# Kernel tuning notes

Measured on AMD Instinct MI355X. Metric: run time of the kernel, lower is better.

## Reference

```python
import jax, jax.numpy as jnp
import numpy as np


def _bilinear(x, py, px):
    # x: [B,C,H,W]; py,px: [B,K,Ho,Wo] fractional sample coords (zero pad outside)
    B, C, H, W = x.shape
    K, Ho, Wo = py.shape[1], py.shape[2], py.shape[3]
    xf = x.reshape(B, C, H * W)
    y0 = jnp.floor(py)
    x0 = jnp.floor(px)

    def gather(yi, xi):
        valid = (yi >= 0) & (yi <= H - 1) & (xi >= 0) & (xi <= W - 1)
        yc = jnp.clip(yi, 0, H - 1).astype(jnp.int32)
        xc = jnp.clip(xi, 0, W - 1).astype(jnp.int32)
        idx = (yc * W + xc).reshape(B, 1, -1)  # [B,1,K*Ho*Wo]
        v = jnp.take_along_axis(xf, idx, axis=2)  # [B,C,K*Ho*Wo]
        return v * valid.reshape(B, 1, -1)

    wy1 = (py - y0).reshape(B, 1, -1)
    wx1 = (px - x0).reshape(B, 1, -1)
    wy0 = 1.0 - wy1
    wx0 = 1.0 - wx1
    v = (gather(y0, x0) * (wy0 * wx0)
         + gather(y0, x0 + 1) * (wy0 * wx1)
         + gather(y0 + 1, x0) * (wy1 * wx0)
         + gather(y0 + 1, x0 + 1) * (wy1 * wx1))
    return v.reshape(B, C, K, Ho, Wo)


def _deform_merge(x, w_off, b_off, w_def, gamma, beta):
    B, C, H, W = x.shape
    Co = w_def.shape[0]
    K, stride = 4, 2  # 2x2 kernel
    Ho, Wo = H // 2, W // 2
    # offset-predicting conv (same k/s/p as deform conv): [B, 2K, Ho, Wo]
    off = jax.lax.conv_general_dilated(x, w_off, (stride, stride), 'VALID')
    off = off + b_off[None, :, None, None]
    off = off.reshape(B, K, 2, Ho, Wo)  # (dy, dx) per kernel tap
    ky = jnp.arange(K) // 2
    kx = jnp.arange(K) % 2
    base_y = (jnp.arange(Ho) * stride)[None, None, :, None] + ky[None, :, None, None]
    base_x = (jnp.arange(Wo) * stride)[None, None, None, :] + kx[None, :, None, None]
    py = base_y.astype(x.dtype) + off[:, :, 0]
    px = base_x.astype(x.dtype) + off[:, :, 1]
    sampled = _bilinear(x, py, px)  # [B,C,K,Ho,Wo]
    y = jnp.einsum('bckhw,ock->bohw', sampled, w_def.reshape(Co, C, K))
    # BatchNorm2d (training-mode batch stats, eps=1e-5) + exact GELU
    mu = y.mean(axis=(0, 2, 3), keepdims=True)
    var = y.var(axis=(0, 2, 3), keepdims=True)
    yn = (y - mu) * jax.lax.rsqrt(var + 1e-5)
    yn = yn * gamma[None, :, None, None] + beta[None, :, None, None]
    yg = jax.nn.gelu(yn, approximate=False)
    return yg.reshape(B, Co, Ho * Wo).transpose(0, 2, 1)  # [B, L/4, Co]


def setup_inputs() -> dict:
    key = jax.random.key(0)
    k0, k1, k2 = jax.random.split(key, 3)
    B, C, H, W, Co = 16, 96, 112, 112, 192
    x = jax.random.normal(k0, (B, C, H, W), jnp.float32)
    # conv_offset: 2*kh*kw = 8 output channels (zero-init in mmcv; small random here)
    w_off = jax.random.normal(k1, (8, C, 2, 2), jnp.float32) * 0.01
    b_off = jnp.zeros((8,), jnp.float32)
    w_def = jax.random.normal(k2, (Co, C, 2, 2), jnp.float32) * (1.0 / np.sqrt(C * 4))
    gamma = jnp.ones((Co,), jnp.float32)
    beta = jnp.zeros((Co,), jnp.float32)
    return {"x": x, "h": H, "w": W, "w_off": w_off, "b_off": b_off,
            "w_def": w_def, "gamma": gamma, "beta": beta}


def reference(x, h, w, w_off, b_off, w_def, gamma, beta):
    assert x.shape[2] == h and x.shape[3] == w
    return _deform_merge(x, w_off, b_off, w_def, gamma, beta)
```

## Files before the change

### kernel.cpp

```cpp
#include <hip/hip_runtime.h>
#include <math.h>

#define BB 16
#define CC 96
#define HH 112
#define WW 112
#define HO 56
#define WO 56
#define LL (HO*WO)
#define CO 192
#define CKD 384
#define NPIX (BB*LL)

#define TPX 28
#define CHK 8
#define NCHUNK 12
#define WROWS 4
#define WCOLS 64
#define WSTRIDE 260
#define APAD 40
#define OSTRIDE 228

#define WS_SSUM  16
#define WS_SSQS  208
#define WS_B_OFF 4096
#define B_ELEMS  73728
#define WS_SOFF_OFF 299008
#define SOFF_BYTES (BB*HO*WO*8*4)

typedef short bf16x8 __attribute__((ext_vector_type(8)));
typedef float f32x4  __attribute__((ext_vector_type(4)));

__device__ __forceinline__ void split8(const float4 a0, const float4 a1,
                                       bf16x8& hi, bf16x8& lo)
{
    float f[8] = {a0.x, a0.y, a0.z, a0.w, a1.x, a1.y, a1.z, a1.w};
    #pragma unroll
    for (int j = 0; j < 8; ++j) {
        unsigned bits = __float_as_uint(f[j]);
        float fh = __uint_as_float(bits & 0xFFFF0000u);
        float fl = f[j] - fh;
        hi[j] = (short)(bits >> 16);
        lo[j] = (short)(__float_as_uint(fl) >> 16);
    }
}

__global__ void k_zero(float* __restrict__ ws) {
    int t = threadIdx.x;
    if (t < 384) ws[WS_SSUM + t] = 0.f;
}

__global__ void k_prep(const float* __restrict__ w_def,
                       unsigned short* __restrict__ bhi,
                       unsigned short* __restrict__ blo,
                       float* __restrict__ ws)
{
    if (blockIdx.x == 0 && threadIdx.x < 384) ws[WS_SSUM + threadIdx.x] = 0.f;
    int t = blockIdx.x * 256 + threadIdx.x;
    if (t >= 12 * 12 * 64) return;
    int ln  = t & 63;
    int ks  = (t >> 6) % 12;
    int ntg = t / (64 * 12);
    int n  = ntg * 16 + (ln & 15);
    int k0 = ks * 32 + (ln >> 4) * 8;
    const float* wp = w_def + (size_t)n * CKD + k0;
    #pragma unroll
    for (int j = 0; j < 8; ++j) {
        float f = wp[j];
        unsigned bits = __float_as_uint(f);
        float fh = __uint_as_float(bits & 0xFFFF0000u);
        float fl = f - fh;
        bhi[t * 8 + j] = (unsigned short)(bits >> 16);
        blo[t * 8 + j] = (unsigned short)(__float_as_uint(fl) >> 16);
    }
}

__global__ __launch_bounds__(512) void k_pre(
    const float* __restrict__ x, const float* __restrict__ w_off,
    const float* __restrict__ b_off, const float* __restrict__ w_def,
    unsigned short* __restrict__ bhi, unsigned short* __restrict__ blo,
    float* __restrict__ soff_all, float* __restrict__ ws)
{
    __shared__ float win[CHK * OSTRIDE];
    const int blk = blockIdx.x;
    const int tid = threadIdx.x;

    if (blk < 18) {
        if (blk == 0 && tid < 384) ws[WS_SSUM + tid] = 0.f;
        int t = blk * 512 + tid;
        int ln  = t & 63;
        int ks  = (t >> 6) % 12;
        int ntg = t / (64 * 12);
        int n  = ntg * 16 + (ln & 15);
        int k0 = ks * 32 + (ln >> 4) * 8;
        const float* wp = w_def + (size_t)n * CKD + k0;
        #pragma unroll
        for (int j = 0; j < 8; ++j) {
            float f = wp[j];
            unsigned bits = __float_as_uint(f);
            float fh = __uint_as_float(bits & 0xFFFF0000u);
            float fl = f - fh;
            bhi[t * 8 + j] = (unsigned short)(bits >> 16);
            blo[t * 8 + j] = (unsigned short)(__float_as_uint(fl) >> 16);
        }
        return;
    }

    const int bb = blk - 18;
    const int oy = bb % HO;
    const int b  = bb / HO;
    const int iy = oy * 2;
    const int pix = tid >> 3, och = tid & 7;
    const int c_s = tid / 56, u_s = tid % 56;
    const int r_s = u_s / 28, q_s = u_s % 28;
    float dacc = 0.f;

    float4 v0, v1, v2;
    #define OFF_LD(CH) (*(const float4*)(x + (((size_t)(b*CC + (CH)*CHK + c_s)*HH) + iy + r_s)*WW + q_s*4))
    if (tid < 448) { v0 = OFF_LD(0); v1 = OFF_LD(1); v2 = OFF_LD(2); }

    #define OFF_STEP(CH, VB) \
        __syncthreads(); \
        if (tid < 448) { \
            *(float4*)&win[c_s*OSTRIDE + r_s*112 + q_s*4] = VB; \
            if ((CH) + 3 < NCHUNK) VB = OFF_LD((CH) + 3); \
        } \
        __syncthreads(); \
        if (tid < 448) { \
            const float* wb = w_off + (size_t)och*(CC*4) + (CH)*CHK*4; \
            _Pragma("unroll") \
            for (int c = 0; c < CHK; ++c) { \
                float2 t0 = *(const float2*)&win[c*OSTRIDE + 2*pix]; \
                float2 t1 = *(const float2*)&win[c*OSTRIDE + 112 + 2*pix]; \
                float4 a = *(const float4*)(wb + c*4); \
                dacc += t0.x*a.x + t0.y*a.y + t1.x*a.z + t1.y*a.w; \
            } \
        }

    #pragma unroll
    for (int g = 0; g < 4; ++g) {
        OFF_STEP(3*g + 0, v0)
        OFF_STEP(3*g + 1, v1)
        OFF_STEP(3*g + 2, v2)
    }
    #undef OFF_STEP
    #undef OFF_LD

    if (tid < 448)
        soff_all[((size_t)(b*HO + oy)*WO)*8 + tid] = dacc + b_off[och];
}

__global__ __launch_bounds__(512, 8) void k_main8(
    const float* __restrict__ x,
    const unsigned short* __restrict__ bhi, const unsigned short* __restrict__ blo,
    const float* __restrict__ soff_all,
    float* __restrict__ yout, float* __restrict__ ws)
{
    __shared__ float win[CHK * WSTRIDE];
    __shared__ unsigned short smAh[32 * APAD];
    __shared__ unsigned short smAl[32 * APAD];
    __shared__ float soff[TPX * 8];

    const int tid = threadIdx.x;
    const int b  = blockIdx.y;
    const int bx = blockIdx.x;
    const int oy  = bx >> 1;
    const int ox0 = (bx & 1) * TPX;
    const int iy  = oy * 2;
    const int ix0 = ox0 * 2;
    const int ln = tid & 63;
    const int w  = tid >> 6;
    const int wr = w & 1;
    const int wc = w >> 1;
    const int row0 = ln & 15;
    const int kg   = ln >> 4;

    if (tid < 128) {
        int rr = 28 + (tid >> 5), cc = tid & 31;
        smAh[rr*APAD + cc] = 0;
        smAl[rr*APAD + cc] = 0;
    }
    if (tid < 56) {
        const float* sp = soff_all + ((size_t)(b*HO + oy)*WO + ox0)*8;
        *(float4*)&soff[tid*4] = *(const float4*)(sp + tid*4);
    }

    const int cg  = tid & 15;
    const int pr  = tid >> 4;
    const int sr  = pr & 3;
    const int scn = pr >> 2;
    const int skk = tid & 31;
    const int sc  = skk >> 2;
    const int sk  = skk & 3;
    const int sky = sk >> 1, skx = sk & 1;
    const int wr0 = iy - 1, wc0 = ix0 - 4;

    auto stage_ld = [&](int ch) -> float4 {
        int gr = min(max(wr0 + sr, 0), HH - 1);
        int gc0 = wc0 + cg * 4;
        const float* src = x + (((size_t)(b*CC + ch*CHK + scn)*HH) + gr)*WW;
        float4 v;
        if (gc0 >= 0 && gc0 <= WW - 4) {
            v = *(const float4*)(src + gc0);
        } else {
            v.x = src[min(max(gc0 + 0, 0), WW - 1)];
            v.y = src[min(max(gc0 + 1, 0), WW - 1)];
            v.z = src[min(max(gc0 + 2, 0), WW - 1)];
            v.w = src[min(max(gc0 + 3, 0), WW - 1)];
        }
        return v;
    };
    float* wdst = &win[scn*WSTRIDE + sr*WCOLS + cg*4];

    f32x4 acc[3];
    #pragma unroll
    for (int nt = 0; nt < 3; ++nt) acc[nt] = (f32x4){0.f, 0.f, 0.f, 0.f};

    float4 vst = stage_ld(NCHUNK - 1);
    *(float4*)wdst = vst;
    vst = stage_ld(NCHUNK - 2);

    for (int ch = NCHUNK - 1; ch >= 0; --ch) {
        __syncthreads();
        {
            const float* xc = x + ((size_t)(b*CC + ch*CHK + sc)*HH)*WW;
            const float* wchan = &win[sc*WSTRIDE];
            #pragma unroll
            for (int j = 0; j < 2; ++j) {
                int pix = (tid >> 5) + 16 * j;
                if (pix < TPX) {
                    float2 so = *(const float2*)&soff[pix*8 + 2*sk];
                    float fy = (float)(iy + sky) + so.x;
                    float fx = (float)(ix0 + 2*pix + skx) + so.y;
                    float y0f = floorf(fy), x0f = floorf(fx);
                    int y0 = (int)y0f, x0 = (int)x0f;
                    float wy1 = fy - y0f, wx1 = fx - x0f;
                    float wy0 = 1.f - wy1, wx0 = 1.f - wx1;
                    int y1 = y0 + 1, x1 = x0 + 1;
                    bool vy0 = (y0 >= 0) && (y0 <= HH - 1);
                    bool vy1 = (y1 >= 0) && (y1 <= HH - 1);
                    bool vx0 = (x0 >= 0) && (x0 <= WW - 1);
                    bool vx1 = (x1 >= 0) && (x1 <= WW - 1);
                    int cy0 = min(max(y0, 0), HH - 1), cy1 = min(max(y1, 0), HH - 1);
                    int cx0 = min(max(x0, 0), WW - 1), cx1 = min(max(x1, 0), WW - 1);
                    float w00 = (vy0 && vx0) ? wy0 * wx0 : 0.f;
                    float w01 = (vy0 && vx1) ? wy0 * wx1 : 0.f;
                    float w10 = (vy1 && vx0) ? wy1 * wx0 : 0.f;
                    float w11 = (vy1 && vx1) ? wy1 * wx1 : 0.f;
                    int ry0 = cy0 - wr0, ry1 = cy1 - wr0;
                    int rx0 = cx0 - wc0, rx1 = cx1 - wc0;
                    bool inw = ((unsigned)ry0 <= (unsigned)(WROWS - 1)) &&
                               ((unsigned)ry1 <= (unsigned)(WROWS - 1)) &&
                               ((unsigned)rx0 <= (unsigned)(WCOLS - 1)) &&
                               ((unsigned)rx1 <= (unsigned)(WCOLS - 1));
                    float v;
                    if (inw) {
                        v = w00 * wchan[ry0*WCOLS + rx0] + w01 * wchan[ry0*WCOLS + rx1]
                          + w10 * wchan[ry1*WCOLS + rx0] + w11 * wchan[ry1*WCOLS + rx1];
                    } else {
                        v = w00 * xc[cy0*WW + cx0] + w01 * xc[cy0*WW + cx1]
                          + w10 * xc[cy1*WW + cx0] + w11 * xc[cy1*WW + cx1];
                    }
                    unsigned u = __float_as_uint(v);
                    float fh = __uint_as_float(u & 0xFFFF0000u);
                    smAh[pix*APAD + skk] = (unsigned short)(u >> 16);
                    smAl[pix*APAD + skk] = (unsigned short)(__float_as_uint(v - fh) >> 16);
                }
            }
        }
        __syncthreads();
        bf16x8 ah = *(const bf16x8*)&smAh[(wr*16 + row0)*APAD + kg*8];
        bf16x8 al = *(const bf16x8*)&smAl[(wr*16 + row0)*APAD + kg*8];
        #pragma unroll
        for (int nt = 0; nt < 3; ++nt) {
            size_t idx = ((size_t)(((wc*3 + nt)*12 + ch)*64) + ln)*8;
            bf16x8 bh = *(const bf16x8*)(bhi + idx);
            bf16x8 bl = *(const bf16x8*)(blo + idx);
            acc[nt] = __builtin_amdgcn_mfma_f32_16x16x32_bf16(ah, bh, acc[nt], 0, 0, 0);
            acc[nt] = __builtin_amdgcn_mfma_f32_16x16x32_bf16(ah, bl, acc[nt], 0, 0, 0);
            acc[nt] = __builtin_amdgcn_mfma_f32_16x16x32_bf16(al, bh, acc[nt], 0, 0, 0);
        }
        if (ch > 0) *(float4*)wdst = vst;
        if (ch > 1) vst = stage_ld(ch - 2);
    }

    #pragma unroll
    for (int nt = 0; nt < 3; ++nt) {
        float s = 0.f, q = 0.f;
        #pragma unroll
        for (int r = 0; r < 4; ++r) {
            float v = acc[nt][r];
            s += v; q += v * v;
        }
        s += __shfl_xor(s, 16); s += __shfl_xor(s, 32);
        q += __shfl_xor(q, 16); q += __shfl_xor(q, 32);
        if (ln < 16) {
            atomicAdd(&ws[WS_SSUM + wc*48 + nt*16 + ln], s);
            atomicAdd(&ws[WS_SSQS + wc*48 + nt*16 + ln], q);
        }
    }
    size_t obase = (size_t)b * LL + (size_t)oy * WO + ox0;
    #pragma unroll
    for (int r = 0; r < 4; ++r) {
        int pp = wr*16 + kg*4 + r;
        if (pp < TPX) {
            float* dst = yout + (obase + pp)*CO + wc*48 + row0;
            dst[0]  = acc[0][r];
            dst[16] = acc[1][r];
            dst[32] = acc[2][r];
        }
    }
}

template<bool PREP>
__device__ __forceinline__ void tile_body(
    const float* __restrict__ x, const float* __restrict__ w_off,
    const float* __restrict__ b_off, const float* __restrict__ w_def,
    const unsigned short* __restrict__ bhi, const unsigned short* __restrict__ blo,
    float* win, unsigned short* smAh, unsigned short* smAl, float* soff,
    int b, int bx, int tid, f32x4 (&acc)[2][3])
{
    const int oy  = bx >> 1;
    const int ox0 = (bx & 1) * TPX;
    const int iy  = oy * 2;
    const int ix0 = ox0 * 2;
    const int ln = tid & 63;
    const int w  = tid >> 6;

    float dacc = 0.f;
    const int cpix = tid >> 3;
    const int coch = tid & 7;
    const int spair = tid / 14;
    const int sq    = tid % 14;
    for (int ch = 0; ch < NCHUNK; ++ch) {
        __syncthreads();
        if (tid < 224) {
            int c = spair >> 1, r = spair & 1;
            const float* src = x + (((size_t)(b*CC + ch*CHK + c)*HH) + iy + r)*WW + ix0 + sq*4;
            *(float4*)&win[(c*2 + r)*56 + sq*4] = *(const float4*)src;
        }
        __syncthreads();
        if (tid < 224) {
            const float* wb = w_off + (size_t)coch*(CC*4) + ch*CHK*4;
            #pragma unroll
            for (int c = 0; c < CHK; ++c) {
                float2 t0 = *(const float2*)&win[(c*2 + 0)*56 + 2*cpix];
                float2 t1 = *(const float2*)&win[(c*2 + 1)*56 + 2*cpix];
                float4 a = *(const float4*)(wb + c*4);
                dacc += t0.x*a.x + t0.y*a.y + t1.x*a.z + t1.y*a.w;
            }
        }
    }
    if (tid < 224) soff[cpix*8 + coch] = dacc + b_off[coch];

    const int row0 = ln & 15;
    const int kg   = ln >> 4;
    const int skk = tid & 31;
    const int sc  = skk >> 2;
    const int sk  = skk & 3;
    const int sky = sk >> 1, skx = sk & 1;
    const int wr0 = iy - 1, wc0 = ix0 - 4;

    for (int ch = NCHUNK - 1; ch >= 0; --ch) {
        __syncthreads();
        #pragma unroll
        for (int j = 0; j < 2; ++j) {
            int li = tid + 256*j;
            int cg = li & 15;
            int pr = li >> 4;
            int r = pr & 3, c = pr >> 2;
            int gr = min(max(wr0 + r, 0), HH - 1);
            int gc0 = wc0 + cg*4;
            const float* src = x + (((size_t)(b*CC + ch*CHK + c)*HH) + gr)*WW;
            float4 v;
            if (gc0 >= 0 && gc0 <= WW - 4) {
                v = *(const float4*)(src + gc0);
            } else {
                v.x = src[min(max(gc0 + 0, 0), WW - 1)];
                v.y = src[min(max(gc0 + 1, 0), WW - 1)];
                v.z = src[min(max(gc0 + 2, 0), WW - 1)];
                v.w = src[min(max(gc0 + 3, 0), WW - 1)];
            }
            *(float4*)&win[c*WSTRIDE + r*WCOLS + cg*4] = v;
        }
        __syncthreads();
        {
            const float* xc = x + ((size_t)(b*CC + ch*CHK + sc)*HH)*WW;
            const float* wchan = &win[sc*WSTRIDE];
            #pragma unroll
            for (int j = 0; j < 4; ++j) {
                if (j < 3 || tid < 128) {
                    int pix = (tid >> 5) + 8*j;
                    float2 so = *(const float2*)&soff[pix*8 + 2*sk];
                    float fy = (float)(iy + sky) + so.x;
                    float fx = (float)(ix0 + 2*pix + skx) + so.y;
                    float y0f = floorf(fy), x0f = floorf(fx);
                    int y0 = (int)y0f, x0 = (int)x0f;
                    float wy1 = fy - y0f, wx1 = fx - x0f;
                    float wy0 = 1.f - wy1, wx0 = 1.f - wx1;
                    int y1 = y0 + 1, x1 = x0 + 1;
                    bool vy0 = (y0 >= 0) && (y0 <= HH - 1);
                    bool vy1 = (y1 >= 0) && (y1 <= HH - 1);
                    bool vx0 = (x0 >= 0) && (x0 <= WW - 1);
                    bool vx1 = (x1 >= 0) && (x1 <= WW - 1);
                    int cy0 = min(max(y0, 0), HH - 1), cy1 = min(max(y1, 0), HH - 1);
                    int cx0 = min(max(x0, 0), WW - 1), cx1 = min(max(x1, 0), WW - 1);
                    float w00 = (vy0 && vx0) ? wy0*wx0 : 0.f;
                    float w01 = (vy0 && vx1) ? wy0*wx1 : 0.f;
                    float w10 = (vy1 && vx0) ? wy1*wx0 : 0.f;
                    float w11 = (vy1 && vx1) ? wy1*wx1 : 0.f;
                    int ry0 = cy0 - wr0, ry1 = cy1 - wr0;
                    int rx0 = cx0 - wc0, rx1 = cx1 - wc0;
                    bool inw = ((unsigned)ry0 <= (unsigned)(WROWS - 1)) &&
                               ((unsigned)ry1 <= (unsigned)(WROWS - 1)) &&
                               ((unsigned)rx0 <= (unsigned)(WCOLS - 1)) &&
                               ((unsigned)rx1 <= (unsigned)(WCOLS - 1));
                    float v;
                    if (inw) {
                        v = w00*wchan[ry0*WCOLS + rx0] + w01*wchan[ry0*WCOLS + rx1]
                          + w10*wchan[ry1*WCOLS + rx0] + w11*wchan[ry1*WCOLS + rx1];
                    } else {
                        v = w00*xc[cy0*WW + cx0] + w01*xc[cy0*WW + cx1]
                          + w10*xc[cy1*WW + cx0] + w11*xc[cy1*WW + cx1];
                    }
                    unsigned u = __float_as_uint(v);
                    float fh = __uint_as_float(u & 0xFFFF0000u);
                    smAh[pix*APAD + skk] = (unsigned short)(u >> 16);
                    smAl[pix*APAD + skk] = (unsigned short)(__float_as_uint(v - fh) >> 16);
                }
            }
        }
        __syncthreads();
        bf16x8 ah[2], al[2];
        #pragma unroll
        for (int mt = 0; mt < 2; ++mt) {
            ah[mt] = *(const bf16x8*)&smAh[(mt*16 + row0)*APAD + kg*8];
            al[mt] = *(const bf16x8*)&smAl[(mt*16 + row0)*APAD + kg*8];
        }
        #pragma unroll
        for (int nt = 0; nt < 3; ++nt) {
            bf16x8 bh, bl;
            if (PREP) {
                size_t idx = ((size_t)(((w*3 + nt)*12 + ch)*64) + ln)*8;
                bh = *(const bf16x8*)(bhi + idx);
                bl = *(const bf16x8*)(blo + idx);
            } else {
                const float* wp = w_def + (size_t)(w*48 + nt*16 + row0)*CKD + ch*32 + kg*8;
                float4 b0 = *(const float4*)wp;
                float4 b1 = *(const float4*)(wp + 4);
                split8(b0, b1, bh, bl);
            }
            #pragma unroll
            for (int mt = 0; mt < 2; ++mt) {
                acc[mt][nt] = __builtin_amdgcn_mfma_f32_16x16x32_bf16(ah[mt], bh, acc[mt][nt], 0, 0, 0);
                acc[mt][nt] = __builtin_amdgcn_mfma_f32_16x16x32_bf16(ah[mt], bl, acc[mt][nt], 0, 0, 0);
                acc[mt][nt] = __builtin_amdgcn_mfma_f32_16x16x32_bf16(al[mt], bh, acc[mt][nt], 0, 0, 0);
            }
        }
    }
}

template<bool PREP>
__global__ __launch_bounds__(256, 4) void k_main_r3(
    const float* __restrict__ x, const float* __restrict__ w_off,
    const float* __restrict__ b_off, const float* __restrict__ w_def,
    const unsigned short* __restrict__ bhi, const unsigned short* __restrict__ blo,
    float* __restrict__ yout, float* __restrict__ ws)
{
    __shared__ float win[CHK * WSTRIDE];
    __shared__ unsigned short smAh[32 * APAD];
    __shared__ unsigned short smAl[32 * APAD];
    __shared__ float soff[TPX * 8];

    const int tid = threadIdx.x;
    const int b  = blockIdx.y;
    const int bx = blockIdx.x;
    const int ln = tid & 63;
    const int w  = tid >> 6;
    const int row0 = ln & 15;
    const int kg   = ln >> 4;

    if (tid < 128) {
        int rr = 28 + (tid >> 5), cc = tid & 31;
        smAh[rr*APAD + cc] = 0;
        smAl[rr*APAD + cc] = 0;
    }

    f32x4 acc[2][3];
    #pragma unroll
    for (int mt = 0; mt < 2; ++mt)
        #pragma unroll
        for (int nt = 0; nt < 3; ++nt)
            acc[mt][nt] = (f32x4){0.f, 0.f, 0.f, 0.f};

    tile_body<PREP>(x, w_off, b_off, w_def, bhi, blo,
                    win, smAh, smAl, soff, b, bx, tid, acc);

    #pragma unroll
    for (int nt = 0; nt < 3; ++nt) {
        float s = 0.f, q = 0.f;
        #pragma unroll
        for (int mt = 0; mt < 2; ++mt)
            #pragma unroll
            for (int r = 0; r < 4; ++r) {
                float v = acc[mt][nt][r];
                s += v; q += v * v;
            }
        s += __shfl_xor(s, 16); s += __shfl_xor(s, 32);
        q += __shfl_xor(q, 16); q += __shfl_xor(q, 32);
        if (ln < 16) {
            atomicAdd(&ws[WS_SSUM + w*48 + nt*16 + ln], s);
            atomicAdd(&ws[WS_SSQS + w*48 + nt*16 + ln], q);
        }
    }
    int oy = bx >> 1, ox0 = (bx & 1)*TPX;
    size_t obase = (size_t)b*LL + (size_t)oy*WO + ox0;
    #pragma unroll
    for (int mt = 0; mt < 2; ++mt)
        #pragma unroll
        for (int r = 0; r < 4; ++r) {
            int pp = mt*16 + kg*4 + r;
            if (pp < TPX) {
                float* dst = yout + (obase + pp)*CO + w*48 + row0;
                dst[0]  = acc[mt][0][r];
                dst[16] = acc[mt][1][r];
                dst[32] = acc[mt][2][r];
            }
        }
}

__global__ __launch_bounds__(256) void k_bn_gelu(
    float* __restrict__ out,
    const float* __restrict__ gamma,
    const float* __restrict__ beta,
    const float* __restrict__ ws)
{
    __shared__ float ssc[CO], ssh[CO];
    int t = threadIdx.x;
    if (t < CO) {
        float n = (float)NPIX;
        float mu = ws[WS_SSUM + t] / n;
        float var = ws[WS_SSQS + t] / n - mu * mu;
        float sc = gamma[t] * rsqrtf(fmaxf(var, 0.f) + 1e-5f);
        ssc[t] = sc;
        ssh[t] = beta[t] - mu * sc;
    }
    __syncthreads();
    long long i4 = ((long long)blockIdx.x * 256 + t) * 4;
    if (i4 >= (long long)NPIX * CO) return;
    int o0 = (int)(i4 % CO);
    float4* p = (float4*)(out + i4);
    float4 v = *p;
    float f[4] = { v.x, v.y, v.z, v.w };
    #pragma unroll
    for (int j = 0; j < 4; ++j) {
        float z = ssc[o0 + j] * f[j] + ssh[o0 + j];
        f[j] = 0.5f * z * (1.f + erff(z * 0.70710678118654752f));
    }
    v.x = f[0]; v.y = f[1]; v.z = f[2]; v.w = f[3];
    *p = v;
}

extern "C" void kernel_launch(void* const* d_in, const int* in_sizes, int n_in,
                              void* d_out, int out_size, void* d_ws, size_t ws_size,
                              hipStream_t stream)
{
    const float *x = nullptr, *w_off = nullptr, *b_off = nullptr;
    const float *w_def = nullptr, *gamma = nullptr, *beta = nullptr;
    for (int i = 0; i < n_in; ++i) {
        int s = in_sizes[i];
        if      (s == 19267584) x     = (const float*)d_in[i];
        else if (s == 3072)     w_off = (const float*)d_in[i];
        else if (s == 8)        b_off = (const float*)d_in[i];
        else if (s == 73728)    w_def = (const float*)d_in[i];
        else if (s == 192) { if (!gamma) gamma = (const float*)d_in[i];
                             else        beta  = (const float*)d_in[i]; }
    }
    if (!x || !w_off || !b_off || !w_def || !gamma || !beta) {
        x = (const float*)d_in[0]; w_off = (const float*)d_in[3];
        b_off = (const float*)d_in[4]; w_def = (const float*)d_in[5];
        gamma = (const float*)d_in[6]; beta = (const float*)d_in[7];
    }

    float* ws = (float*)d_ws;
    float* out = (float*)d_out;

    unsigned short* bhi = (unsigned short*)((char*)d_ws + WS_B_OFF);
    unsigned short* blo = bhi + B_ELEMS;
    float* soff_all = (float*)((char*)d_ws + WS_SOFF_OFF);
    bool big = ws_size >= (size_t)(WS_SOFF_OFF + SOFF_BYTES);

    if (big) {
        k_pre<<<18 + HO*BB, 512, 0, stream>>>(x, w_off, b_off, w_def, bhi, blo, soff_all, ws);
        k_main8<<<dim3(112, BB), 512, 0, stream>>>(x, bhi, blo, soff_all, out, ws);
    } else {
        bool prep = ws_size >= (size_t)(WS_B_OFF + 2*B_ELEMS*sizeof(unsigned short));
        if (prep) {
            k_prep<<<36, 256, 0, stream>>>(w_def, bhi, blo, ws);
            k_main_r3<true><<<dim3(112, BB), 256, 0, stream>>>(x, w_off, b_off, w_def, bhi, blo, out, ws);
        } else {
            k_zero<<<1, 384, 0, stream>>>(ws);
            k_main_r3<false><<<dim3(112, BB), 256, 0, stream>>>(x, w_off, b_off, w_def, bhi, blo, out, ws);
        }
    }
    k_bn_gelu<<<dim3((int)(((long long)NPIX*CO/4 + 255) / 256)), 256, 0, stream>>>(out, gamma, beta, ws);
}
```

Measured before the change: 347.9 us.

## Simplify offset conv to direct global loads and drop window prefetch pipeline

The offset-prediction kernel no longer stages x through shared memory with triple-buffered register prefetch and barriers. Each thread now computes one (pixel, offset-channel) output directly from global memory over all 96 channels. The main kernel also drops its register prefetch of the next window chunk and instead loads and stores the window synchronously at the top of each chunk iteration, with an extra barrier. This cuts register pressure and barrier count, but loses load/compute overlap and the coalesced loads of the staged version.

```diff
diff --git a/kernel.cpp b/kernel.cpp
--- a/kernel.cpp
+++ b/kernel.cpp
@@ -19,7 +19,6 @@
 #define WCOLS 64
 #define WSTRIDE 260
 #define APAD 40
-#define OSTRIDE 228
 
 #define WS_SSUM  16
 #define WS_SSQS  208
@@ -81,7 +80,6 @@
     unsigned short* __restrict__ bhi, unsigned short* __restrict__ blo,
     float* __restrict__ soff_all, float* __restrict__ ws)
 {
-    __shared__ float win[CHK * OSTRIDE];
     const int blk = blockIdx.x;
     const int tid = threadIdx.x;
 
@@ -110,44 +108,21 @@
     const int oy = bb % HO;
     const int b  = bb / HO;
     const int iy = oy * 2;
-    const int pix = tid >> 3, och = tid & 7;
-    const int c_s = tid / 56, u_s = tid % 56;
-    const int r_s = u_s / 28, q_s = u_s % 28;
+    if (tid >= 448) return;
+    const int och = tid / 56;
+    const int ox  = tid % 56;
+    const float* xb = x + (((size_t)(b * CC) * HH) + iy) * WW + 2 * ox;
+    const float* wb = w_off + (size_t)och * (CC * 4);
     float dacc = 0.f;
-
-    float4 v0, v1, v2;
-    #define OFF_LD(CH) (*(const float4*)(x + (((size_t)(b*CC + (CH)*CHK + c_s)*HH) + iy + r_s)*WW + q_s*4))
-    if (tid < 448) { v0 = OFF_LD(0); v1 = OFF_LD(1); v2 = OFF_LD(2); }
-
-    #define OFF_STEP(CH, VB) \
-        __syncthreads(); \
-        if (tid < 448) { \
-            *(float4*)&win[c_s*OSTRIDE + r_s*112 + q_s*4] = VB; \
-            if ((CH) + 3 < NCHUNK) VB = OFF_LD((CH) + 3); \
-        } \
-        __syncthreads(); \
-        if (tid < 448) { \
-            const float* wb = w_off + (size_t)och*(CC*4) + (CH)*CHK*4; \
-            _Pragma("unroll") \
-            for (int c = 0; c < CHK; ++c) { \
-                float2 t0 = *(const float2*)&win[c*OSTRIDE + 2*pix]; \
-                float2 t1 = *(const float2*)&win[c*OSTRIDE + 112 + 2*pix]; \
-                float4 a = *(const float4*)(wb + c*4); \
-                dacc += t0.x*a.x + t0.y*a.y + t1.x*a.z + t1.y*a.w; \
-            } \
-        }
-
-    #pragma unroll
-    for (int g = 0; g < 4; ++g) {
-        OFF_STEP(3*g + 0, v0)
-        OFF_STEP(3*g + 1, v1)
-        OFF_STEP(3*g + 2, v2)
-    }
-    #undef OFF_STEP
-    #undef OFF_LD
-
-    if (tid < 448)
-        soff_all[((size_t)(b*HO + oy)*WO)*8 + tid] = dacc + b_off[och];
+    #pragma unroll 8
+    for (int c = 0; c < CC; ++c) {
+        const float* xp = xb + (size_t)c * (HH * WW);
+        float2 t0 = *(const float2*)(xp);
+        float2 t1 = *(const float2*)(xp + WW);
+        float4 a  = *(const float4*)(wb + c * 4);
+        dacc += t0.x * a.x + t0.y * a.y + t1.x * a.z + t1.y * a.w;
+    }
+    soff_all[(((size_t)(b * HO + oy) * WO) + ox) * 8 + och] = dacc + b_off[och];
 }
 
 __global__ __launch_bounds__(512, 8) void k_main8(
@@ -195,32 +170,27 @@
     const int sky = sk >> 1, skx = sk & 1;
     const int wr0 = iy - 1, wc0 = ix0 - 4;
 
-    auto stage_ld = [&](int ch) -> float4 {
-        int gr = min(max(wr0 + sr, 0), HH - 1);
-        int gc0 = wc0 + cg * 4;
-        const float* src = x + (((size_t)(b*CC + ch*CHK + scn)*HH) + gr)*WW;
-        float4 v;
-        if (gc0 >= 0 && gc0 <= WW - 4) {
-            v = *(const float4*)(src + gc0);
-        } else {
-            v.x = src[min(max(gc0 + 0, 0), WW - 1)];
-            v.y = src[min(max(gc0 + 1, 0), WW - 1)];
-            v.z = src[min(max(gc0 + 2, 0), WW - 1)];
-            v.w = src[min(max(gc0 + 3, 0), WW - 1)];
-        }
-        return v;
-    };
-    float* wdst = &win[scn*WSTRIDE + sr*WCOLS + cg*4];
-
     f32x4 acc[3];
     #pragma unroll
     for (int nt = 0; nt < 3; ++nt) acc[nt] = (f32x4){0.f, 0.f, 0.f, 0.f};
 
-    float4 vst = stage_ld(NCHUNK - 1);
-    *(float4*)wdst = vst;
-    vst = stage_ld(NCHUNK - 2);
-
     for (int ch = NCHUNK - 1; ch >= 0; --ch) {
+        __syncthreads();
+        {
+            int gr = min(max(wr0 + sr, 0), HH - 1);
+            int gc0 = wc0 + cg * 4;
+            const float* src = x + (((size_t)(b*CC + ch*CHK + scn)*HH) + gr)*WW;
+            float4 v;
+            if (gc0 >= 0 && gc0 <= WW - 4) {
+                v = *(const float4*)(src + gc0);
+            } else {
+                v.x = src[min(max(gc0 + 0, 0), WW - 1)];
+                v.y = src[min(max(gc0 + 1, 0), WW - 1)];
+                v.z = src[min(max(gc0 + 2, 0), WW - 1)];
+                v.w = src[min(max(gc0 + 3, 0), WW - 1)];
+            }
+            *(float4*)&win[scn*WSTRIDE + sr*WCOLS + cg*4] = v;
+        }
         __syncthreads();
         {
             const float* xc = x + ((size_t)(b*CC + ch*CHK + sc)*HH)*WW;
@@ -280,8 +250,6 @@
             acc[nt] = __builtin_amdgcn_mfma_f32_16x16x32_bf16(ah, bl, acc[nt], 0, 0, 0);
             acc[nt] = __builtin_amdgcn_mfma_f32_16x16x32_bf16(al, bh, acc[nt], 0, 0, 0);
         }
-        if (ch > 0) *(float4*)wdst = vst;
-        if (ch > 1) vst = stage_ld(ch - 2);
     }
 
     #pragma unroll
```

Result: faster. 339.0 us (-2.6%).
